# Kernel tuning notes

Hardware: AMD Instinct MI355X
Metric: run time of the kernel (lower is better)

Reference implementation:

```python
import jax, jax.numpy as jnp
import numpy as np

B, S, IN, OUT = 4, 2048, 4096, 16384

def setup_inputs() -> dict:
    key = jax.random.key(0)
    k1, k2, k3, k4 = jax.random.split(key, 4)
    x = jax.random.normal(k1, (B, S, IN), dtype=jnp.float32)
    quantized_weight = jax.random.randint(k2, (OUT, IN), 0, 16, dtype=jnp.int32)
    scale = jax.random.uniform(k3, (OUT,), dtype=jnp.float32)
    zero_point = jax.random.randint(k4, (OUT,), 0, 16, dtype=jnp.int32)
    return {"x": x, "quantized_weight": quantized_weight, "scale": scale, "zero_point": zero_point}

def reference(x, quantized_weight, scale, zero_point):
    # Per-output-channel dequantization: W = (q - zp) * scale, shape [OUT, IN]
    weight = (quantized_weight.astype(jnp.float32) - zero_point.astype(jnp.float32)[:, None]) * scale[:, None]
    # F.linear(x, W) = x @ W.T -> [B, S, OUT]
    return jnp.einsum('bsi,oi->bso', x, weight)
```

## Files before the change

kernel.cpp:

```cpp
#include <hip/hip_runtime.h>
#include <stdint.h>

#define MDIM 8192
#define NDIM 16384
#define KDIM 4096
#define NT   64

typedef __attribute__((ext_vector_type(4))) int i32x4;

__device__ __forceinline__ void gload_lds16(const void* g, void* l) {
    __builtin_amdgcn_global_load_lds(
        (const __attribute__((address_space(1))) void*)g,
        (__attribute__((address_space(3))) void*)l,
        16, 0, 0);
}

__device__ __forceinline__ i32x4 MFMA8(i32x4 a, i32x4 b, i32x4 c) {
    return __builtin_amdgcn_mfma_i32_16x16x64_i8(a, b, c, 0, 0, 0);
}


__global__ __launch_bounds__(256)
void quant_x_kernel(const float* __restrict__ x, int8_t* __restrict__ xq,
                    float* __restrict__ sx) {
    const int row = (int)blockIdx.x;
    const float* xr = x + (long)row * KDIM;
    const int t = threadIdx.x;
    float v[16];
#pragma unroll
    for (int i = 0; i < 4; ++i)
        *(float4*)&v[i * 4] = ((const float4*)xr)[t + 256 * i];
    float m = 0.f;
#pragma unroll
    for (int i = 0; i < 16; ++i) m = fmaxf(m, fabsf(v[i]));
#pragma unroll
    for (int off = 32; off >= 1; off >>= 1) m = fmaxf(m, __shfl_xor(m, off));
    __shared__ float red[4];
    if ((t & 63) == 0) red[t >> 6] = m;
    __syncthreads();
    m = fmaxf(fmaxf(red[0], red[1]), fmaxf(red[2], red[3]));
    m = fmaxf(m, 1e-20f);
    const float inv = 127.0f / m;
    if (t == 0) sx[row] = m * (1.0f / 127.0f);
    int* qo = (int*)(xq + (long)row * KDIM);
#pragma unroll
    for (int i = 0; i < 4; ++i) {
        union { int8_t c[4]; int w; } o;
#pragma unroll
        for (int j = 0; j < 4; ++j)
            o.c[j] = (int8_t)__float2int_rn(v[i * 4 + j] * inv);
        qo[t + 256 * i] = o.w;
    }
}

__global__ __launch_bounds__(256)
void quant_w_kernel(const int* __restrict__ q, const int* __restrict__ zp,
                    int8_t* __restrict__ wq) {
    const long i = (long)blockIdx.x * 256 + threadIdx.x;
    const long e = i * 16;
    const int o = (int)(e >> 12);
    const int z = zp[o];
    union { int8_t c[16]; int4 v; } r;
#pragma unroll
    for (int b = 0; b < 4; ++b) {
        int4 a = ((const int4*)(q + e))[b];
        r.c[b * 4 + 0] = (int8_t)(a.x - z);
        r.c[b * 4 + 1] = (int8_t)(a.y - z);
        r.c[b * 4 + 2] = (int8_t)(a.z - z);
        r.c[b * 4 + 3] = (int8_t)(a.w - z);
    }
    *(int4*)(wq + e) = r.v;
}


__global__ __launch_bounds__(512, 2)
void gemm_i8_kernel(const int8_t* __restrict__ A, const int8_t* __restrict__ Wt,
                    const float* __restrict__ scale, const float* __restrict__ sx,
                    float* __restrict__ C) {
    __shared__ int8_t lds[3 * 32768];

    const int wg = (int)blockIdx.x;
    const int rr = wg >> 8;
    const int ii = wg & 255;
    const int bm = ii & 31;
    const int bn = rr * 8 + (ii >> 5);

    const int tid  = threadIdx.x;
    const int lane = tid & 63;
    const int wid  = tid >> 6;
    const int wm   = wid >> 2;
    const int wn   = wid & 3;
    const int l15  = lane & 15;
    const int c16  = lane >> 4;

    const int axor = (l15 >> 1) & 3;
    const int fro  = l15 * 64 + ((c16 ^ axor) << 4);

    const int s0 = tid, s1 = 512 + tid;
    const int soff0 = (s0 >> 2) * KDIM + ((((s0 & 3) ^ ((s0 >> 3) & 3))) << 4);
    const int soff1 = (s1 >> 2) * KDIM + ((((s1 & 3) ^ ((s1 >> 3) & 3))) << 4);
    const int d0 = s0 * 16, d1 = s1 * 16;

    const int8_t* Ab = A  + (long)bm * 256 * KDIM;
    const int8_t* Wb = Wt + (long)bn * 256 * KDIM;

#define STAGE(bb, P, base, tt)                                                      \
    do {                                                                            \
        gload_lds16((base) + soff0 + (tt) * 64, &lds[(bb) + (P) * 16384 + d0]);     \
        gload_lds16((base) + soff1 + (tt) * 64, &lds[(bb) + (P) * 16384 + d1]);     \
    } while (0)

#define RDA(DST, BB, IB)                                                            \
    _Pragma("unroll")                                                               \
    for (int i_ = 0; i_ < 4; ++i_)                                                  \
        DST[i_] = *(const i32x4*)&lds[(BB) + (wm * 128 + ((IB) + i_) * 16) * 64 + fro];

#define RDB(DST, BB)                                                                \
    _Pragma("unroll")                                                               \
    for (int j_ = 0; j_ < 4; ++j_)                                                  \
        DST[j_] = *(const i32x4*)&lds[(BB) + 16384 + (wn * 64 + j_ * 16) * 64 + fro];

#define MFMAQ(IB, AS, BS)                                                           \
    _Pragma("unroll")                                                               \
    for (int i_ = 0; i_ < 4; ++i_)                                                  \
        _Pragma("unroll")                                                           \
        for (int j_ = 0; j_ < 4; ++j_)                                              \
            acc[(IB) + i_][j_] = MFMA8(AS[i_], BS[j_], acc[(IB) + i_][j_]);

    i32x4 acc[8][4];
#pragma unroll
    for (int i = 0; i < 8; ++i)
#pragma unroll
        for (int j = 0; j < 4; ++j) acc[i][j] = (i32x4){0, 0, 0, 0};

    i32x4 aS0[4], aS1[4], bSA[4], bSB[4];
    int b0 = 0, b1 = 32768, b2 = 65536;

    STAGE(b0, 0, Ab, 0); STAGE(b0, 1, Wb, 0);
    STAGE(b1, 0, Ab, 1); STAGE(b1, 1, Wb, 1);
    asm volatile("s_waitcnt vmcnt(4)" ::: "memory");
    __builtin_amdgcn_s_barrier();
    RDA(aS0, b0, 0);
    RDB(bSA, b0);

#define KSTEP(T, BCUR, BNXT)                                                        \
    do {                                                                            \
        const bool pf_ = (T) < NT - 2;                                              \
                            \
        RDA(aS1, b0, 4);                                                            \
        if (pf_) { STAGE(b2, 0, Ab, (T) + 2); }                                     \
        __builtin_amdgcn_sched_barrier(0);                                          \
        __builtin_amdgcn_s_setprio(1);                                              \
        MFMAQ(0, aS0, BCUR);                                                        \
        __builtin_amdgcn_s_setprio(0);                                              \
        __builtin_amdgcn_sched_barrier(0);                                          \
                \
        asm volatile("s_waitcnt lgkmcnt(0)" ::: "memory");                          \
        if (pf_) asm volatile("s_waitcnt vmcnt(2)" ::: "memory");                   \
        else     asm volatile("s_waitcnt vmcnt(0)" ::: "memory");                   \
        __builtin_amdgcn_s_barrier();                                               \
        RDA(aS0, b1, 0);                                                            \
        RDB(BNXT, b1);                                                              \
        if (pf_) { STAGE(b2, 1, Wb, (T) + 2); }                                     \
        __builtin_amdgcn_sched_barrier(0);                                          \
        __builtin_amdgcn_s_setprio(1);                                              \
        MFMAQ(4, aS1, BCUR);                                                        \
        __builtin_amdgcn_s_setprio(0);                                              \
        __builtin_amdgcn_sched_barrier(0);                                          \
        const int tb_ = b0; b0 = b1; b1 = b2; b2 = tb_;                             \
    } while (0)

    for (int t = 0; t < NT; t += 2) {
        KSTEP(t,     bSA, bSB);
        KSTEP(t + 1, bSB, bSA);
    }
#undef KSTEP
#undef STAGE
#undef RDA
#undef RDB
#undef MFMAQ

    const long rowA0 = (long)bm * 256 + wm * 128;
    const int  colB0 = bn * 256 + wn * 64;
    float scj[4];
#pragma unroll
    for (int j = 0; j < 4; ++j) scj[j] = scale[colB0 + j * 16 + l15];
#pragma unroll
    for (int i = 0; i < 8; ++i) {
        const long rbase = rowA0 + i * 16 + c16 * 4;
        const float4 s4 = *(const float4*)(sx + rbase);
#pragma unroll
        for (int j = 0; j < 4; ++j) {
            float* cp = C + rbase * NDIM + colB0 + j * 16 + l15;
            cp[0 * (long)NDIM] = (float)acc[i][j][0] * scj[j] * s4.x;
            cp[1 * (long)NDIM] = (float)acc[i][j][1] * scj[j] * s4.y;
            cp[2 * (long)NDIM] = (float)acc[i][j][2] * scj[j] * s4.z;
            cp[3 * (long)NDIM] = (float)acc[i][j][3] * scj[j] * s4.w;
        }
    }
}


__global__ __launch_bounds__(256)
void fallback_kernel(const float* __restrict__ x, const int* __restrict__ q,
                     const float* __restrict__ scale, const int* __restrict__ zp,
                     float* __restrict__ out) {
    __shared__ float sA[64][17];
    __shared__ float sB[64][17];
    const int bn = (int)blockIdx.x % (NDIM / 64);
    const int bm = (int)blockIdx.x / (NDIM / 64);
    const int t  = threadIdx.x;
    const int tx = t & 15, ty = t >> 4;
    const long rowA = (long)bm * 64, rowB = (long)bn * 64;
    float acc[4][4] = {};
    for (int k0 = 0; k0 < KDIM; k0 += 16) {
#pragma unroll
        for (int i = 0; i < 4; ++i) {
            const int e = t + i * 256;
            const int r = e >> 4, c = e & 15;
            sA[r][c] = x[(rowA + r) * KDIM + k0 + c];
            const int o = (int)rowB + r;
            sB[r][c] = (float)(q[(long)o * KDIM + k0 + c] - zp[o]) * scale[o];
        }
        __syncthreads();
#pragma unroll
        for (int kk = 0; kk < 16; ++kk) {
            float a[4], b[4];
#pragma unroll
            for (int i = 0; i < 4; ++i) a[i] = sA[ty * 4 + i][kk];
#pragma unroll
            for (int j = 0; j < 4; ++j) b[j] = sB[tx * 4 + j][kk];
#pragma unroll
            for (int i = 0; i < 4; ++i)
#pragma unroll
                for (int j = 0; j < 4; ++j) acc[i][j] += a[i] * b[j];
        }
        __syncthreads();
    }
#pragma unroll
    for (int i = 0; i < 4; ++i) {
        const long r = rowA + ty * 4 + i;
#pragma unroll
        for (int j = 0; j < 4; ++j)
            out[r * NDIM + rowB + tx * 4 + j] = acc[i][j];
    }
}


extern "C" void kernel_launch(void* const* d_in, const int* in_sizes, int n_in,
                              void* d_out, int out_size, void* d_ws, size_t ws_size,
                              hipStream_t stream) {
    const float* x     = (const float*)d_in[0];
    const int*   qw    = (const int*)d_in[1];
    const float* scale = (const float*)d_in[2];
    const int*   zp    = (const int*)d_in[3];
    float*       out   = (float*)d_out;

    const size_t needA  = (size_t)MDIM * KDIM;
    const size_t needW  = (size_t)NDIM * KDIM;
    const size_t needSx = (size_t)MDIM * sizeof(float);

    if (ws_size >= needA + needW + needSx) {
        int8_t* xq = (int8_t*)d_ws;
        int8_t* wq = xq + needA;
        float*  sx = (float*)((char*)d_ws + needA + needW);
        quant_x_kernel<<<MDIM, 256, 0, stream>>>(x, xq, sx);
        quant_w_kernel<<<(NDIM * (KDIM / 16)) / 256, 256, 0, stream>>>(qw, zp, wq);
        gemm_i8_kernel<<<(MDIM / 256) * (NDIM / 256), 512, 0, stream>>>(xq, wq, scale, sx, out);
    } else {
        fallback_kernel<<<(MDIM / 64) * (NDIM / 64), 256, 0, stream>>>(x, qw, scale, zp, out);
    }
}
```

Baseline: 684.2 us.

## Ping-pong the two wave groups between LDS reads and MFMA phases

Replaces the per-wave interleaved LDS-read/MFMA K-step with a ping-pong schedule. Each iteration is split into two barrier-separated halves: one wave row group (wm) loads its whole A/B fragment set from LDS while the other runs its full 8x4 MFMA block, and the roles swap in the second half. Global-to-LDS staging is spread across the two halves. The aim is to keep the matrix units busy while LDS traffic from the other group is in flight. In exchange it uses more fragment registers and adds barriers. The fixed vmcnt(4) wait may not cover the last tile when no further prefetch has been issued.

```diff
diff --git a/kernel.cpp b/kernel.cpp
--- a/kernel.cpp
+++ b/kernel.cpp
@@ -110,75 +110,70 @@
         gload_lds16((base) + soff1 + (tt) * 64, &lds[(bb) + (P) * 16384 + d1]);     \
     } while (0)
 
-#define RDA(DST, BB, IB)                                                            \
-    _Pragma("unroll")                                                               \
-    for (int i_ = 0; i_ < 4; ++i_)                                                  \
-        DST[i_] = *(const i32x4*)&lds[(BB) + (wm * 128 + ((IB) + i_) * 16) * 64 + fro];
-
-#define RDB(DST, BB)                                                                \
-    _Pragma("unroll")                                                               \
-    for (int j_ = 0; j_ < 4; ++j_)                                                  \
-        DST[j_] = *(const i32x4*)&lds[(BB) + 16384 + (wn * 64 + j_ * 16) * 64 + fro];
-
-#define MFMAQ(IB, AS, BS)                                                           \
-    _Pragma("unroll")                                                               \
-    for (int i_ = 0; i_ < 4; ++i_)                                                  \
+#define RDALL(BB)                                                                   \
+    do {                                                                            \
+        _Pragma("unroll")                                                           \
+        for (int i_ = 0; i_ < 8; ++i_)                                              \
+            aF[i_] = *(const i32x4*)&lds[(BB) + (wm * 128 + i_ * 16) * 64 + fro];   \
         _Pragma("unroll")                                                           \
         for (int j_ = 0; j_ < 4; ++j_)                                              \
-            acc[(IB) + i_][j_] = MFMA8(AS[i_], BS[j_], acc[(IB) + i_][j_]);
-
-    i32x4 acc[8][4];
-#pragma unroll
-    for (int i = 0; i < 8; ++i)
-#pragma unroll
-        for (int j = 0; j < 4; ++j) acc[i][j] = (i32x4){0, 0, 0, 0};
-
-    i32x4 aS0[4], aS1[4], bSA[4], bSB[4];
-    int b0 = 0, b1 = 32768, b2 = 65536;
-
-    STAGE(b0, 0, Ab, 0); STAGE(b0, 1, Wb, 0);
-    STAGE(b1, 0, Ab, 1); STAGE(b1, 1, Wb, 1);
-    asm volatile("s_waitcnt vmcnt(4)" ::: "memory");
-    __builtin_amdgcn_s_barrier();
-    RDA(aS0, b0, 0);
-    RDB(bSA, b0);
-
-#define KSTEP(T, BCUR, BNXT)                                                        \
+            bF[j_] = *(const i32x4*)&lds[(BB) + 16384 + (wn * 64 + j_ * 16) * 64 + fro]; \
+    } while (0)
+
+#define MFMAALL()                                                                   \
     do {                                                                            \
-        const bool pf_ = (T) < NT - 2;                                              \
-                            \
-        RDA(aS1, b0, 4);                                                            \
-        if (pf_) { STAGE(b2, 0, Ab, (T) + 2); }                                     \
         __builtin_amdgcn_sched_barrier(0);                                          \
         __builtin_amdgcn_s_setprio(1);                                              \
-        MFMAQ(0, aS0, BCUR);                                                        \
+        _Pragma("unroll")                                                           \
+        for (int i_ = 0; i_ < 8; ++i_)                                              \
+            _Pragma("unroll")                                                       \
+            for (int j_ = 0; j_ < 4; ++j_)                                          \
+                acc[i_][j_] = MFMA8(aF[i_], bF[j_], acc[i_][j_]);                   \
         __builtin_amdgcn_s_setprio(0);                                              \
         __builtin_amdgcn_sched_barrier(0);                                          \
-                \
-        asm volatile("s_waitcnt lgkmcnt(0)" ::: "memory");                          \
-        if (pf_) asm volatile("s_waitcnt vmcnt(2)" ::: "memory");                   \
-        else     asm volatile("s_waitcnt vmcnt(0)" ::: "memory");                   \
-        __builtin_amdgcn_s_barrier();                                               \
-        RDA(aS0, b1, 0);                                                            \
-        RDB(BNXT, b1);                                                              \
-        if (pf_) { STAGE(b2, 1, Wb, (T) + 2); }                                     \
-        __builtin_amdgcn_sched_barrier(0);                                          \
-        __builtin_amdgcn_s_setprio(1);                                              \
-        MFMAQ(4, aS1, BCUR);                                                        \
-        __builtin_amdgcn_s_setprio(0);                                              \
-        __builtin_amdgcn_sched_barrier(0);                                          \
-        const int tb_ = b0; b0 = b1; b1 = b2; b2 = tb_;                             \
     } while (0)
 
-    for (int t = 0; t < NT; t += 2) {
-        KSTEP(t,     bSA, bSB);
-        KSTEP(t + 1, bSB, bSA);
-    }
-#undef KSTEP
+    i32x4 acc[8][4];
+#pragma unroll
+    for (int i = 0; i < 8; ++i)
+#pragma unroll
+        for (int j = 0; j < 4; ++j) acc[i][j] = (i32x4){0, 0, 0, 0};
+
+    i32x4 aF[8], bF[4];
+
+    int cb = 0, nb = 32768, fb = 65536;
+    STAGE(cb, 0, Ab, 0); STAGE(cb, 1, Wb, 0);
+    STAGE(nb, 0, Ab, 1); STAGE(nb, 1, Wb, 1);
+
+    for (int t = 0; t < NT; ++t) {
+        const bool st = (t + 2 < NT);
+
+        asm volatile("s_waitcnt lgkmcnt(0)" ::: "memory");
+        asm volatile("s_waitcnt vmcnt(4)" ::: "memory");
+        __builtin_amdgcn_s_barrier();
+        if (st) STAGE(fb, 0, Ab, t + 2);
+        if (wm == 0) {
+            RDALL(cb);
+        } else if (t > 0) {
+            MFMAALL();
+        }
+
+        asm volatile("s_waitcnt lgkmcnt(0)" ::: "memory");
+        __builtin_amdgcn_s_barrier();
+        if (st) STAGE(fb, 1, Wb, t + 2);
+        if (wm == 1) {
+            RDALL(cb);
+        } else {
+            MFMAALL();
+        }
+
+        const int tmp = cb; cb = nb; nb = fb; fb = tmp;
+    }
+    if (wm == 1) MFMAALL();
+
 #undef STAGE
-#undef RDA
-#undef RDB
-#undef MFMAQ
+#undef RDALL
+#undef MFMAALL
 
     const long rowA0 = (long)bm * 256 + wm * 128;
     const int  colB0 = bn * 256 + wn * 64;
```

New measurement: 679.0 us. About the same (-0.8%).
